# Kernel optimization log

Hardware: AMD Instinct MI355X
Metric: run time of the kernel (lower is better)

Reference implementation:

```python
import jax, jax.numpy as jnp
import numpy as np

N_NODES = 100000
N_EDGES = 1200000
N_GRAPHS = 1024
IN_FEATS = 64
HID = 64
BN_EPS = 1e-5


def setup_inputs() -> dict:
    key = jax.random.key(0)
    ks = jax.random.split(key, 20)
    feats = jax.random.normal(ks[0], (N_NODES, IN_FEATS), jnp.float32)
    src = jax.random.randint(ks[1], (N_EDGES,), 0, N_NODES, jnp.int32)
    dst = jax.random.randint(ks[2], (N_EDGES,), 0, N_NODES, jnp.int32)
    graph_ids = jnp.sort(jax.random.randint(ks[3], (N_NODES,), 0, N_GRAPHS, jnp.int32))

    def lin(k, fi, fo):
        s = 1.0 / np.sqrt(fi)
        kw, kb = jax.random.split(k)
        return (jax.random.uniform(kw, (fi, fo), jnp.float32, -s, s),
                jax.random.uniform(kb, (fo,), jnp.float32, -s, s))

    W_self, _ = lin(ks[4], IN_FEATS, HID)
    W_neigh, b_neigh = lin(ks[5], IN_FEATS, HID)
    W1, b1 = lin(ks[6], HID, 128)
    W2, b2 = lin(ks[7], 128, 64)
    W3, b3 = lin(ks[8], 64, 1)

    def bn(k, d):
        k1, k2, k3, k4 = jax.random.split(k, 4)
        return (jax.random.normal(k1, (d,), jnp.float32) * 0.1 + 1.0,
                jax.random.normal(k2, (d,), jnp.float32) * 0.1,
                jax.random.normal(k3, (d,), jnp.float32) * 0.1,
                jax.random.uniform(k4, (d,), jnp.float32, 0.5, 1.5))

    g1, be1, rm1, rv1 = bn(ks[9], 128)
    g2, be2, rm2, rv2 = bn(ks[10], 64)

    return dict(feats=feats, src=src, dst=dst, graph_ids=graph_ids,
                W_self=W_self, W_neigh=W_neigh, b_neigh=b_neigh,
                W1=W1, b1=b1, g1=g1, be1=be1, rm1=rm1, rv1=rv1,
                W2=W2, b2=b2, g2=g2, be2=be2, rm2=rm2, rv2=rv2,
                W3=W3, b3=b3)


def reference(feats, src, dst, graph_ids, W_self, W_neigh, b_neigh,
              W1, b1, g1, be1, rm1, rv1, W2, b2, g2, be2, rm2, rv2, W3, b3):
    # --- SAGEConv (mean aggregator): h = W_self@h_self + W_neigh@mean_neigh + b
    deg = jax.ops.segment_sum(jnp.ones((src.shape[0],), feats.dtype), dst,
                              num_segments=N_NODES)                      # [N]
    agg = jax.ops.segment_sum(feats[src], dst, num_segments=N_NODES)     # [N, F]
    mean_neigh = agg / jnp.maximum(deg, 1.0)[:, None]
    h = feats @ W_self + mean_neigh @ W_neigh + b_neigh
    h = jax.nn.relu(h)                                                   # activation

    # --- per-graph max readout (dgl.max_nodes)
    hg = jax.ops.segment_max(h, graph_ids, num_segments=N_GRAPHS)        # [G, HID]

    # --- MLP head with eval-mode BatchNorm1d
    def bn(x, g, b, rm, rv):
        return (x - rm) * jax.lax.rsqrt(rv + BN_EPS) * g + b

    x = bn(jax.nn.relu(hg @ W1 + b1), g1, be1, rm1, rv1)
    x = bn(jax.nn.relu(x @ W2 + b2), g2, be2, rm2, rv2)
    return x @ W3 + b3                                                   # [G, n_task]
```

## Files before the change

### kernel.cpp

```cpp
#include <hip/hip_runtime.h>
#include <hip/hip_fp16.h>

#define N_NODES  100000
#define N_EDGES  1200000
#define N_GRAPHS 1024
#define F        64
#define BN_EPS   1e-5f
#define NBUCK    ((N_NODES + 255) / 256)
#define NBLK     512
#define CHUNK    ((N_EDGES + NBLK - 1) / NBLK)
#define MT       128

__global__ __launch_bounds__(256) void chist(const int* __restrict__ dst,
                                             int* __restrict__ Ct,
                                             int* __restrict__ hgbits) {
  __shared__ int lh[NBUCK];
  int b = blockIdx.x, t = threadIdx.x;
  int zidx = b * 256 + t;
  if (zidx < N_GRAPHS * F) hgbits[zidx] = 0;
  for (int i = t; i < NBUCK; i += 256) lh[i] = 0;
  __syncthreads();
  int e0 = b * CHUNK, e1 = e0 + CHUNK;
  if (e1 > N_EDGES) e1 = N_EDGES;
  for (int e = e0 + t; e < e1; e += 256) atomicAdd(&lh[dst[e] >> 8], 1);
  __syncthreads();
  for (int i = t; i < NBUCK; i += 256) Ct[(size_t)b * NBUCK + i] = lh[i];
}

__global__ __launch_bounds__(NBLK) void cscan(int* __restrict__ Ct,
                                              int* __restrict__ bcnt) {
  __shared__ int s[NBLK];
  int i = blockIdx.x, t = threadIdx.x;
  int v = Ct[(size_t)t * NBUCK + i];
  s[t] = v;
  __syncthreads();
  for (int off = 1; off < NBLK; off <<= 1) {
    int u = (t >= off) ? s[t - off] : 0;
    __syncthreads();
    s[t] += u;
    __syncthreads();
  }
  Ct[(size_t)t * NBUCK + i] = s[t] - v;
  if (t == NBLK - 1) bcnt[i] = s[NBLK - 1];
}

__global__ __launch_bounds__(512) void bscan(const int* __restrict__ bcnt,
                                             int* __restrict__ bstart) {
  __shared__ int s[512];
  int t = threadIdx.x;
  int v = (t < NBUCK) ? bcnt[t] : 0;
  s[t] = v;
  __syncthreads();
  for (int off = 1; off < 512; off <<= 1) {
    int u = (t >= off) ? s[t - off] : 0;
    __syncthreads();
    s[t] += u;
    __syncthreads();
  }
  if (t < NBUCK) bstart[t] = s[t] - v;
  if (t == 0) bstart[NBUCK] = N_EDGES;
}

__global__ __launch_bounds__(256) void cscat(const int* __restrict__ src,
                                             const int* __restrict__ dst,
                                             const int* __restrict__ Ct,
                                             const int* __restrict__ bstart,
                                             int* __restrict__ pairs) {
  __shared__ int cur[NBUCK];
  int b = blockIdx.x, t = threadIdx.x;
  for (int i = t; i < NBUCK; i += 256)
    cur[i] = bstart[i] + Ct[(size_t)b * NBUCK + i];
  __syncthreads();
  int e0 = b * CHUNK, e1 = e0 + CHUNK;
  if (e1 > N_EDGES) e1 = N_EDGES;
  for (int e = e0 + t; e < e1; e += 256) {
    int d = dst[e];
    int pos = atomicAdd(&cur[d >> 8], 1);
    pairs[pos] = (int)((((unsigned)d & 255u) << 24) | (unsigned)src[e]);
  }
}

__global__ __launch_bounds__(256) void place(const int* __restrict__ pairs,
                                             const int* __restrict__ bstart,
                                             int* __restrict__ rs,
                                             int* __restrict__ eidx) {
  __shared__ int lh[256];
  __shared__ int cur[256];
  int b = blockIdx.x, t = threadIdx.x;
  int nb0 = b << 8;
  int r0 = bstart[b], r1 = bstart[b + 1];

  lh[t] = 0;
  __syncthreads();
  for (int e = r0 + t; e < r1; e += 256)
    atomicAdd(&lh[((unsigned)pairs[e]) >> 24], 1);
  __syncthreads();

  int v = lh[t];
  cur[t] = v;
  __syncthreads();
  for (int off = 1; off < 256; off <<= 1) {
    int u = (t >= off) ? cur[t - off] : 0;
    __syncthreads();
    cur[t] += u;
    __syncthreads();
  }
  int excl = cur[t] - v;
  int node = nb0 + t;
  if (node < N_NODES) rs[node] = r0 + excl;
  if (b == 0 && t == 0) rs[N_NODES] = N_EDGES;
  __syncthreads();
  cur[t] = r0 + excl;
  __syncthreads();

  for (int e = r0 + t; e < r1; e += 256) {
    unsigned p = (unsigned)pairs[e];
    int pos = atomicAdd(&cur[p >> 24], 1);
    eidx[pos] = (int)(p & 0xFFFFFFu);
  }
}

__global__ __launch_bounds__(256) void gemm_uz(
    const float* __restrict__ feats, const float* __restrict__ Wself,
    const float* __restrict__ Wneigh, __half* __restrict__ Uh,
    __half* __restrict__ Zh) {
  __shared__ float As[MT * 65];
  __shared__ float Ws[64 * 128];
  int t = threadIdx.x;
  int mbase = blockIdx.x * MT;

  for (int i = t; i < 64 * 128; i += 256) {
    int k = i >> 7, j = i & 127;
    Ws[i] = (j < 64) ? Wself[k * 64 + j] : Wneigh[k * 64 + (j - 64)];
  }
#pragma unroll
  for (int s = 0; s < 8; s++) {
    int idx = (s * 256 + t) * 4;
    int m = idx >> 6, k = idx & 63;
    int gm = mbase + m;
    float4 v = (gm < N_NODES) ? *(const float4*)(feats + (size_t)gm * F + k)
                              : make_float4(0.f, 0.f, 0.f, 0.f);
    float* d = As + m * 65 + k;
    d[0] = v.x; d[1] = v.y; d[2] = v.z; d[3] = v.w;
  }
  __syncthreads();

  int wave = t >> 6, lane = t & 63;
  int jq = lane & 3, nq = lane >> 2;
  int half = wave & 1;
  int mb = (wave >> 1) * 64 + 4 * nq;
  int joff = half * 64 + jq * 16;

  float acc[4][16];
#pragma unroll
  for (int i = 0; i < 4; i++)
#pragma unroll
    for (int c = 0; c < 16; c++) acc[i][c] = 0.f;

#pragma unroll 4
  for (int k = 0; k < 64; k++) {
    float a0 = As[(mb + 0) * 65 + k];
    float a1 = As[(mb + 1) * 65 + k];
    float a2 = As[(mb + 2) * 65 + k];
    float a3 = As[(mb + 3) * 65 + k];
    const float4* wr = (const float4*)(Ws + k * 128 + joff);
    float4 w4[4];
    w4[0] = wr[0]; w4[1] = wr[1]; w4[2] = wr[2]; w4[3] = wr[3];
    const float* w = (const float*)w4;
#pragma unroll
    for (int c = 0; c < 16; c++) {
      float wv = w[c];
      acc[0][c] += a0 * wv;
      acc[1][c] += a1 * wv;
      acc[2][c] += a2 * wv;
      acc[3][c] += a3 * wv;
    }
  }

  __half* outp = half ? Zh : Uh;
  int jbase = jq * 16;
#pragma unroll
  for (int i = 0; i < 4; i++) {
    int gm = mbase + mb + i;
    if (gm < N_NODES) {
#pragma unroll
      for (int c4 = 0; c4 < 4; c4++) {
        union { __half h[4]; uint2 u; } pk;
        pk.h[0] = __float2half_rn(acc[i][c4 * 4 + 0]);
        pk.h[1] = __float2half_rn(acc[i][c4 * 4 + 1]);
        pk.h[2] = __float2half_rn(acc[i][c4 * 4 + 2]);
        pk.h[3] = __float2half_rn(acc[i][c4 * 4 + 3]);
        *(uint2*)(outp + (size_t)gm * F + jbase + c4 * 4) = pk.u;
      }
    }
  }
}

__global__ __launch_bounds__(256) void gather_h(
    const __half* __restrict__ Uh, const __half* __restrict__ Zh,
    const int* __restrict__ rs, const int* __restrict__ eidx,
    const float* __restrict__ bneigh, const int* __restrict__ gids,
    int* __restrict__ hgbits) {
  int lane = threadIdx.x & 63;
  int wid  = (blockIdx.x * blockDim.x + threadIdx.x) >> 6;
  const int NW = (2048 * 256) >> 6;
  const int per = (N_NODES + NW - 1) / NW;
  int n0 = wid * per;
  int n1 = n0 + per; if (n1 > N_NODES) n1 = N_NODES;
  if (n0 >= n1) return;
  int fl  = lane & 15;
  int sub = lane >> 4;
  float4 b4 = *(const float4*)(bneigh + 4 * fl);

  int curg = gids[n0];
  float4 gmax = {0.f, 0.f, 0.f, 0.f};

  for (int n = n0; n < n1; n++) {
    uint2 ur = *(const uint2*)(Uh + (size_t)n * F + 4 * fl);
    int r0 = rs[n], r1 = rs[n + 1];
    float sx = 0.f, sy = 0.f, sz = 0.f, sw = 0.f;
    for (int base = r0; base < r1; base += 64) {
      int m = r1 - base; if (m > 64) m = 64;
      int myid = (lane < m) ? eidx[base + lane] : 0;
      for (int jj = 0; jj < m; jj += 16) {
        int j0 = jj + sub;
        int s0 = __shfl(myid, j0);
        int s1 = __shfl(myid, j0 + 4);
        int s2 = __shfl(myid, j0 + 8);
        int s3 = __shfl(myid, j0 + 12);
        uint2 z0 = *(const uint2*)(Zh + (size_t)s0 * F + 4 * fl);
        uint2 z1 = *(const uint2*)(Zh + (size_t)s1 * F + 4 * fl);
        uint2 z2 = *(const uint2*)(Zh + (size_t)s2 * F + 4 * fl);
        uint2 z3 = *(const uint2*)(Zh + (size_t)s3 * F + 4 * fl);
        if (j0 < m) {
          float2 f0 = __half22float2(*(__half2*)&z0.x);
          float2 f1 = __half22float2(*(__half2*)&z0.y);
          sx += f0.x; sy += f0.y; sz += f1.x; sw += f1.y;
        }
        if (j0 + 4 < m) {
          float2 f0 = __half22float2(*(__half2*)&z1.x);
          float2 f1 = __half22float2(*(__half2*)&z1.y);
          sx += f0.x; sy += f0.y; sz += f1.x; sw += f1.y;
        }
        if (j0 + 8 < m) {
          float2 f0 = __half22float2(*(__half2*)&z2.x);
          float2 f1 = __half22float2(*(__half2*)&z2.y);
          sx += f0.x; sy += f0.y; sz += f1.x; sw += f1.y;
        }
        if (j0 + 12 < m) {
          float2 f0 = __half22float2(*(__half2*)&z3.x);
          float2 f1 = __half22float2(*(__half2*)&z3.y);
          sx += f0.x; sy += f0.y; sz += f1.x; sw += f1.y;
        }
      }
    }
    sx += __shfl_xor(sx, 16); sy += __shfl_xor(sy, 16);
    sz += __shfl_xor(sz, 16); sw += __shfl_xor(sw, 16);
    sx += __shfl_xor(sx, 32); sy += __shfl_xor(sy, 32);
    sz += __shfl_xor(sz, 32); sw += __shfl_xor(sw, 32);
    float inv = 1.0f / fmaxf((float)(r1 - r0), 1.0f);

    int g = gids[n];
    if (g != curg) {
      if (sub == 0) {
        int* hp = hgbits + (size_t)curg * F + 4 * fl;
        atomicMax(hp + 0, __float_as_int(gmax.x));
        atomicMax(hp + 1, __float_as_int(gmax.y));
        atomicMax(hp + 2, __float_as_int(gmax.z));
        atomicMax(hp + 3, __float_as_int(gmax.w));
      }
      curg = g; gmax = make_float4(0.f, 0.f, 0.f, 0.f);
    }

    float2 uf0 = __half22float2(*(__half2*)&ur.x);
    float2 uf1 = __half22float2(*(__half2*)&ur.y);
    gmax.x = fmaxf(gmax.x, fmaxf(uf0.x + sx * inv + b4.x, 0.f));
    gmax.y = fmaxf(gmax.y, fmaxf(uf0.y + sy * inv + b4.y, 0.f));
    gmax.z = fmaxf(gmax.z, fmaxf(uf1.x + sz * inv + b4.z, 0.f));
    gmax.w = fmaxf(gmax.w, fmaxf(uf1.y + sw * inv + b4.w, 0.f));
  }
  if (sub == 0) {
    int* hp = hgbits + (size_t)curg * F + 4 * fl;
    atomicMax(hp + 0, __float_as_int(gmax.x));
    atomicMax(hp + 1, __float_as_int(gmax.y));
    atomicMax(hp + 2, __float_as_int(gmax.z));
    atomicMax(hp + 3, __float_as_int(gmax.w));
  }
}

#define GPB 8
__global__ __launch_bounds__(128) void mlp(
    const float* __restrict__ hg,
    const float* __restrict__ W1, const float* __restrict__ b1,
    const float* __restrict__ g1, const float* __restrict__ be1,
    const float* __restrict__ rm1, const float* __restrict__ rv1,
    const float* __restrict__ W2, const float* __restrict__ b2,
    const float* __restrict__ g2, const float* __restrict__ be2,
    const float* __restrict__ rm2, const float* __restrict__ rv2,
    const float* __restrict__ W3, const float* __restrict__ b3,
    float* __restrict__ out) {
  __shared__ float W1s[64 * 128];
  __shared__ float W2s[128 * 64];
  __shared__ float W3s[64];
  __shared__ float sc1[128], sh1[128], b1s[128];
  __shared__ float sc2[64],  sh2[64],  b2s[64];
  __shared__ float s0[64], s1[128], s2[64];
  int t = threadIdx.x;

  for (int i = t; i < 64 * 128; i += 128) W1s[i] = W1[i];
  for (int i = t; i < 128 * 64; i += 128) W2s[i] = W2[i];
  if (t < 64) W3s[t] = W3[t];
  {
    float iv = rsqrtf(rv1[t] + BN_EPS);
    float sc = g1[t] * iv;
    sc1[t] = sc; sh1[t] = be1[t] - rm1[t] * sc; b1s[t] = b1[t];
  }
  if (t < 64) {
    float iv = rsqrtf(rv2[t] + BN_EPS);
    float sc = g2[t] * iv;
    sc2[t] = sc; sh2[t] = be2[t] - rm2[t] * sc; b2s[t] = b2[t];
  }
  __syncthreads();

  for (int gg = 0; gg < GPB; gg++) {
    int g = blockIdx.x * GPB + gg;
    if (t < 64) s0[t] = hg[(size_t)g * F + t];
    __syncthreads();
    {
      float acc = b1s[t];
      for (int i = 0; i < 64; i++) acc += s0[i] * W1s[i * 128 + t];
      acc = fmaxf(acc, 0.0f);
      s1[t] = acc * sc1[t] + sh1[t];
    }
    __syncthreads();
    if (t < 64) {
      float acc = b2s[t];
      for (int i = 0; i < 128; i++) acc += s1[i] * W2s[i * 64 + t];
      acc = fmaxf(acc, 0.0f);
      s2[t] = acc * sc2[t] + sh2[t];
    }
    __syncthreads();
    if (t < 64) {
      float p = s2[t] * W3s[t];
      for (int off = 32; off > 0; off >>= 1) p += __shfl_down(p, off);
      if (t == 0) out[g] = p + b3[0];
    }
    __syncthreads();
  }
}

extern "C" void kernel_launch(void* const* d_in, const int* in_sizes, int n_in,
                              void* d_out, int out_size, void* d_ws, size_t ws_size,
                              hipStream_t stream) {
  const float* feats  = (const float*)d_in[0];
  const int*   src    = (const int*)d_in[1];
  const int*   dst    = (const int*)d_in[2];
  const int*   gids   = (const int*)d_in[3];
  const float* Wself  = (const float*)d_in[4];
  const float* Wneigh = (const float*)d_in[5];
  const float* bneigh = (const float*)d_in[6];
  const float* W1  = (const float*)d_in[7];
  const float* b1  = (const float*)d_in[8];
  const float* g1  = (const float*)d_in[9];
  const float* be1 = (const float*)d_in[10];
  const float* rm1 = (const float*)d_in[11];
  const float* rv1 = (const float*)d_in[12];
  const float* W2  = (const float*)d_in[13];
  const float* b2  = (const float*)d_in[14];
  const float* g2  = (const float*)d_in[15];
  const float* be2 = (const float*)d_in[16];
  const float* rm2 = (const float*)d_in[17];
  const float* rv2 = (const float*)d_in[18];
  const float* W3  = (const float*)d_in[19];
  const float* b3  = (const float*)d_in[20];

  __half* Uh   = (__half*)d_ws;
  __half* Zh   = Uh + (size_t)N_NODES * F;
  int* rs      = (int*)(Zh + (size_t)N_NODES * F);
  int* bstart  = rs + (N_NODES + 1);
  int* bcnt    = bstart + (NBUCK + 1);
  int* hgbits  = bcnt + NBUCK;
  int* Ct      = hgbits + (size_t)N_GRAPHS * F;
  int* pairs   = Ct + (size_t)NBLK * NBUCK;
  int* eidx    = pairs + N_EDGES;

  chist<<<NBLK, 256, 0, stream>>>(dst, Ct, hgbits);
  cscan<<<NBUCK, NBLK, 0, stream>>>(Ct, bcnt);
  bscan<<<1, 512, 0, stream>>>(bcnt, bstart);
  cscat<<<NBLK, 256, 0, stream>>>(src, dst, Ct, bstart, pairs);
  gemm_uz<<<(N_NODES + MT - 1) / MT, 256, 0, stream>>>(feats, Wself, Wneigh,
                                                       Uh, Zh);
  place<<<NBUCK, 256, 0, stream>>>(pairs, bstart, rs, eidx);
  gather_h<<<2048, 256, 0, stream>>>(Uh, Zh, rs, eidx, bneigh, gids, hgbits);
  mlp<<<N_GRAPHS / GPB, 128, 0, stream>>>((const float*)hgbits,
                                          W1, b1, g1, be1, rm1, rv1,
                                          W2, b2, g2, be2, rm2, rv2, W3, b3,
                                          (float*)d_out);
}
```

Before: 230.1 us.

## Fuse histogram into GEMM launch, merge scans, prefetch edge ids in gather

Adds the destination histogram blocks to the GEMM launch as extra blocks and merges the column scan with the bucket scan, using a last-block-done counter. This cuts two kernel launches and lets the histogram run alongside the GEMM. The gather kernel now loads the next node's row bounds and first 64 edge ids before finishing the current node, and it launches with twice as many blocks. This adds a threadfence and atomic counter plus extra registers, and the shared-memory buffer is sized for the GEMM, which may lower occupancy for the histogram blocks.

New measurement: 303.1 us. 1.32x slower.

```diff
diff --git a/kernel.cpp b/kernel.cpp
--- a/kernel.cpp
+++ b/kernel.cpp
@@ -10,123 +10,34 @@
 #define NBLK     512
 #define CHUNK    ((N_EDGES + NBLK - 1) / NBLK)
 #define MT       128
-
-__global__ __launch_bounds__(256) void chist(const int* __restrict__ dst,
-                                             int* __restrict__ Ct,
-                                             int* __restrict__ hgbits) {
-  __shared__ int lh[NBUCK];
-  int b = blockIdx.x, t = threadIdx.x;
-  int zidx = b * 256 + t;
-  if (zidx < N_GRAPHS * F) hgbits[zidx] = 0;
-  for (int i = t; i < NBUCK; i += 256) lh[i] = 0;
-  __syncthreads();
-  int e0 = b * CHUNK, e1 = e0 + CHUNK;
-  if (e1 > N_EDGES) e1 = N_EDGES;
-  for (int e = e0 + t; e < e1; e += 256) atomicAdd(&lh[dst[e] >> 8], 1);
-  __syncthreads();
-  for (int i = t; i < NBUCK; i += 256) Ct[(size_t)b * NBUCK + i] = lh[i];
-}
-
-__global__ __launch_bounds__(NBLK) void cscan(int* __restrict__ Ct,
-                                              int* __restrict__ bcnt) {
-  __shared__ int s[NBLK];
-  int i = blockIdx.x, t = threadIdx.x;
-  int v = Ct[(size_t)t * NBUCK + i];
-  s[t] = v;
-  __syncthreads();
-  for (int off = 1; off < NBLK; off <<= 1) {
-    int u = (t >= off) ? s[t - off] : 0;
-    __syncthreads();
-    s[t] += u;
-    __syncthreads();
-  }
-  Ct[(size_t)t * NBUCK + i] = s[t] - v;
-  if (t == NBLK - 1) bcnt[i] = s[NBLK - 1];
-}
-
-__global__ __launch_bounds__(512) void bscan(const int* __restrict__ bcnt,
-                                             int* __restrict__ bstart) {
-  __shared__ int s[512];
-  int t = threadIdx.x;
-  int v = (t < NBUCK) ? bcnt[t] : 0;
-  s[t] = v;
-  __syncthreads();
-  for (int off = 1; off < 512; off <<= 1) {
-    int u = (t >= off) ? s[t - off] : 0;
-    __syncthreads();
-    s[t] += u;
-    __syncthreads();
-  }
-  if (t < NBUCK) bstart[t] = s[t] - v;
-  if (t == 0) bstart[NBUCK] = N_EDGES;
-}
-
-__global__ __launch_bounds__(256) void cscat(const int* __restrict__ src,
-                                             const int* __restrict__ dst,
-                                             const int* __restrict__ Ct,
-                                             const int* __restrict__ bstart,
-                                             int* __restrict__ pairs) {
-  __shared__ int cur[NBUCK];
-  int b = blockIdx.x, t = threadIdx.x;
-  for (int i = t; i < NBUCK; i += 256)
-    cur[i] = bstart[i] + Ct[(size_t)b * NBUCK + i];
-  __syncthreads();
-  int e0 = b * CHUNK, e1 = e0 + CHUNK;
-  if (e1 > N_EDGES) e1 = N_EDGES;
-  for (int e = e0 + t; e < e1; e += 256) {
-    int d = dst[e];
-    int pos = atomicAdd(&cur[d >> 8], 1);
-    pairs[pos] = (int)((((unsigned)d & 255u) << 24) | (unsigned)src[e]);
-  }
-}
-
-__global__ __launch_bounds__(256) void place(const int* __restrict__ pairs,
-                                             const int* __restrict__ bstart,
-                                             int* __restrict__ rs,
-                                             int* __restrict__ eidx) {
-  __shared__ int lh[256];
-  __shared__ int cur[256];
-  int b = blockIdx.x, t = threadIdx.x;
-  int nb0 = b << 8;
-  int r0 = bstart[b], r1 = bstart[b + 1];
-
-  lh[t] = 0;
-  __syncthreads();
-  for (int e = r0 + t; e < r1; e += 256)
-    atomicAdd(&lh[((unsigned)pairs[e]) >> 24], 1);
-  __syncthreads();
-
-  int v = lh[t];
-  cur[t] = v;
-  __syncthreads();
-  for (int off = 1; off < 256; off <<= 1) {
-    int u = (t >= off) ? cur[t - off] : 0;
-    __syncthreads();
-    cur[t] += u;
-    __syncthreads();
-  }
-  int excl = cur[t] - v;
-  int node = nb0 + t;
-  if (node < N_NODES) rs[node] = r0 + excl;
-  if (b == 0 && t == 0) rs[N_NODES] = N_EDGES;
-  __syncthreads();
-  cur[t] = r0 + excl;
-  __syncthreads();
-
-  for (int e = r0 + t; e < r1; e += 256) {
-    unsigned p = (unsigned)pairs[e];
-    int pos = atomicAdd(&cur[p >> 24], 1);
-    eidx[pos] = (int)(p & 0xFFFFFFu);
-  }
-}
-
-__global__ __launch_bounds__(256) void gemm_uz(
+#define GEMM_BLOCKS ((N_NODES + MT - 1) / MT)
+
+__global__ __launch_bounds__(256) void prep(
     const float* __restrict__ feats, const float* __restrict__ Wself,
     const float* __restrict__ Wneigh, __half* __restrict__ Uh,
-    __half* __restrict__ Zh) {
-  __shared__ float As[MT * 65];
-  __shared__ float Ws[64 * 128];
+    __half* __restrict__ Zh, const int* __restrict__ dst,
+    int* __restrict__ Ct, int* __restrict__ hgbits, int* __restrict__ done) {
+  __shared__ __align__(16) char smraw[MT * 65 * 4 + 64 * 128 * 4];
   int t = threadIdx.x;
+  if (blockIdx.x == 0 && t == 0) *done = 0;
+
+  if (blockIdx.x >= GEMM_BLOCKS) {
+    int* lh = (int*)smraw;
+    int b = blockIdx.x - GEMM_BLOCKS;
+    int zidx = b * 256 + t;
+    if (zidx < N_GRAPHS * F) hgbits[zidx] = 0;
+    for (int i = t; i < NBUCK; i += 256) lh[i] = 0;
+    __syncthreads();
+    int e0 = b * CHUNK, e1 = e0 + CHUNK;
+    if (e1 > N_EDGES) e1 = N_EDGES;
+    for (int e = e0 + t; e < e1; e += 256) atomicAdd(&lh[dst[e] >> 8], 1);
+    __syncthreads();
+    for (int i = t; i < NBUCK; i += 256) Ct[(size_t)b * NBUCK + i] = lh[i];
+    return;
+  }
+
+  float* As = (float*)smraw;
+  float* Ws = (float*)(smraw + MT * 65 * 4);
   int mbase = blockIdx.x * MT;
 
   for (int i = t; i < 64 * 128; i += 256) {
@@ -196,6 +107,102 @@
   }
 }
 
+__global__ __launch_bounds__(NBLK) void cscan2(int* __restrict__ Ct,
+                                               int* __restrict__ bcnt,
+                                               int* __restrict__ bstart,
+                                               int* __restrict__ done) {
+  __shared__ int s[NBLK];
+  __shared__ int lastflag;
+  int i = blockIdx.x, t = threadIdx.x;
+  int v = Ct[(size_t)t * NBUCK + i];
+  s[t] = v;
+  __syncthreads();
+  for (int off = 1; off < NBLK; off <<= 1) {
+    int u = (t >= off) ? s[t - off] : 0;
+    __syncthreads();
+    s[t] += u;
+    __syncthreads();
+  }
+  Ct[(size_t)t * NBUCK + i] = s[t] - v;
+  if (t == NBLK - 1) bcnt[i] = s[NBLK - 1];
+  __threadfence();
+  __syncthreads();
+  if (t == 0) lastflag = (atomicAdd(done, 1) == NBUCK - 1) ? 1 : 0;
+  __syncthreads();
+  if (!lastflag) return;
+
+  int w = (t < NBUCK) ? atomicAdd(&bcnt[t], 0) : 0;
+  s[t] = w;
+  __syncthreads();
+  for (int off = 1; off < NBLK; off <<= 1) {
+    int u = (t >= off) ? s[t - off] : 0;
+    __syncthreads();
+    s[t] += u;
+    __syncthreads();
+  }
+  if (t < NBUCK) bstart[t] = s[t] - w;
+  if (t == 0) bstart[NBUCK] = N_EDGES;
+}
+
+__global__ __launch_bounds__(256) void cscat(const int* __restrict__ src,
+                                             const int* __restrict__ dst,
+                                             const int* __restrict__ Ct,
+                                             const int* __restrict__ bstart,
+                                             int* __restrict__ pairs) {
+  __shared__ int cur[NBUCK];
+  int b = blockIdx.x, t = threadIdx.x;
+  for (int i = t; i < NBUCK; i += 256)
+    cur[i] = bstart[i] + Ct[(size_t)b * NBUCK + i];
+  __syncthreads();
+  int e0 = b * CHUNK, e1 = e0 + CHUNK;
+  if (e1 > N_EDGES) e1 = N_EDGES;
+  for (int e = e0 + t; e < e1; e += 256) {
+    int d = dst[e];
+    int pos = atomicAdd(&cur[d >> 8], 1);
+    pairs[pos] = (int)((((unsigned)d & 255u) << 24) | (unsigned)src[e]);
+  }
+}
+
+__global__ __launch_bounds__(256) void place(const int* __restrict__ pairs,
+                                             const int* __restrict__ bstart,
+                                             int* __restrict__ rs,
+                                             int* __restrict__ eidx) {
+  __shared__ int lh[256];
+  __shared__ int cur[256];
+  int b = blockIdx.x, t = threadIdx.x;
+  int nb0 = b << 8;
+  int r0 = bstart[b], r1 = bstart[b + 1];
+
+  lh[t] = 0;
+  __syncthreads();
+  for (int e = r0 + t; e < r1; e += 256)
+    atomicAdd(&lh[((unsigned)pairs[e]) >> 24], 1);
+  __syncthreads();
+
+  int v = lh[t];
+  cur[t] = v;
+  __syncthreads();
+  for (int off = 1; off < 256; off <<= 1) {
+    int u = (t >= off) ? cur[t - off] : 0;
+    __syncthreads();
+    cur[t] += u;
+    __syncthreads();
+  }
+  int excl = cur[t] - v;
+  int node = nb0 + t;
+  if (node < N_NODES) rs[node] = r0 + excl;
+  if (b == 0 && t == 0) rs[N_NODES] = N_EDGES;
+  __syncthreads();
+  cur[t] = r0 + excl;
+  __syncthreads();
+
+  for (int e = r0 + t; e < r1; e += 256) {
+    unsigned p = (unsigned)pairs[e];
+    int pos = atomicAdd(&cur[p >> 24], 1);
+    eidx[pos] = (int)(p & 0xFFFFFFu);
+  }
+}
+
 __global__ __launch_bounds__(256) void gather_h(
     const __half* __restrict__ Uh, const __half* __restrict__ Zh,
     const int* __restrict__ rs, const int* __restrict__ eidx,
@@ -203,7 +210,7 @@
     int* __restrict__ hgbits) {
   int lane = threadIdx.x & 63;
   int wid  = (blockIdx.x * blockDim.x + threadIdx.x) >> 6;
-  const int NW = (2048 * 256) >> 6;
+  const int NW = (4096 * 256) >> 6;
   const int per = (N_NODES + NW - 1) / NW;
   int n0 = wid * per;
   int n1 = n0 + per; if (n1 > N_NODES) n1 = N_NODES;
@@ -215,19 +222,57 @@
   int curg = gids[n0];
   float4 gmax = {0.f, 0.f, 0.f, 0.f};
 
+  int r0 = rs[n0], r1 = rs[n0 + 1];
+  int myid = (lane < r1 - r0) ? eidx[r0 + lane] : 0;
+
   for (int n = n0; n < n1; n++) {
     uint2 ur = *(const uint2*)(Uh + (size_t)n * F + 4 * fl);
-    int r0 = rs[n], r1 = rs[n + 1];
+    int nr0 = 0, nr1 = 0;
+    if (n + 1 < n1) { nr0 = rs[n + 1]; nr1 = rs[n + 2]; }
+
     float sx = 0.f, sy = 0.f, sz = 0.f, sw = 0.f;
-    for (int base = r0; base < r1; base += 64) {
+    int deg = r1 - r0;
+    int m0 = deg > 64 ? 64 : deg;
+    for (int jj = 0; jj < m0; jj += 16) {
+      int j0 = jj + sub;
+      int s0 = __shfl(myid, j0);
+      int s1 = __shfl(myid, j0 + 4);
+      int s2 = __shfl(myid, j0 + 8);
+      int s3 = __shfl(myid, j0 + 12);
+      uint2 z0 = *(const uint2*)(Zh + (size_t)s0 * F + 4 * fl);
+      uint2 z1 = *(const uint2*)(Zh + (size_t)s1 * F + 4 * fl);
+      uint2 z2 = *(const uint2*)(Zh + (size_t)s2 * F + 4 * fl);
+      uint2 z3 = *(const uint2*)(Zh + (size_t)s3 * F + 4 * fl);
+      if (j0 < m0) {
+        float2 f0 = __half22float2(*(__half2*)&z0.x);
+        float2 f1 = __half22float2(*(__half2*)&z0.y);
+        sx += f0.x; sy += f0.y; sz += f1.x; sw += f1.y;
+      }
+      if (j0 + 4 < m0) {
+        float2 f0 = __half22float2(*(__half2*)&z1.x);
+        float2 f1 = __half22float2(*(__half2*)&z1.y);
+        sx += f0.x; sy += f0.y; sz += f1.x; sw += f1.y;
+      }
+      if (j0 + 8 < m0) {
+        float2 f0 = __half22float2(*(__half2*)&z2.x);
+        float2 f1 = __half22float2(*(__half2*)&z2.y);
+        sx += f0.x; sy += f0.y; sz += f1.x; sw += f1.y;
+      }
+      if (j0 + 12 < m0) {
+        float2 f0 = __half22float2(*(__half2*)&z3.x);
+        float2 f1 = __half22float2(*(__half2*)&z3.y);
+        sx += f0.x; sy += f0.y; sz += f1.x; sw += f1.y;
+      }
+    }
+    for (int base = r0 + 64; base < r1; base += 64) {
       int m = r1 - base; if (m > 64) m = 64;
-      int myid = (lane < m) ? eidx[base + lane] : 0;
+      int myid2 = (lane < m) ? eidx[base + lane] : 0;
       for (int jj = 0; jj < m; jj += 16) {
         int j0 = jj + sub;
-        int s0 = __shfl(myid, j0);
-        int s1 = __shfl(myid, j0 + 4);
-        int s2 = __shfl(myid, j0 + 8);
-        int s3 = __shfl(myid, j0 + 12);
+        int s0 = __shfl(myid2, j0);
+        int s1 = __shfl(myid2, j0 + 4);
+        int s2 = __shfl(myid2, j0 + 8);
+        int s3 = __shfl(myid2, j0 + 12);
         uint2 z0 = *(const uint2*)(Zh + (size_t)s0 * F + 4 * fl);
         uint2 z1 = *(const uint2*)(Zh + (size_t)s1 * F + 4 * fl);
         uint2 z2 = *(const uint2*)(Zh + (size_t)s2 * F + 4 * fl);
@@ -254,11 +299,15 @@
         }
       }
     }
+
+    int nmyid = 0;
+    if (n + 1 < n1) nmyid = (lane < nr1 - nr0) ? eidx[nr0 + lane] : 0;
+
     sx += __shfl_xor(sx, 16); sy += __shfl_xor(sy, 16);
     sz += __shfl_xor(sz, 16); sw += __shfl_xor(sw, 16);
     sx += __shfl_xor(sx, 32); sy += __shfl_xor(sy, 32);
     sz += __shfl_xor(sz, 32); sw += __shfl_xor(sw, 32);
-    float inv = 1.0f / fmaxf((float)(r1 - r0), 1.0f);
+    float inv = 1.0f / fmaxf((float)deg, 1.0f);
 
     int g = gids[n];
     if (g != curg) {
@@ -278,6 +327,8 @@
     gmax.y = fmaxf(gmax.y, fmaxf(uf0.y + sy * inv + b4.y, 0.f));
     gmax.z = fmaxf(gmax.z, fmaxf(uf1.x + sz * inv + b4.z, 0.f));
     gmax.w = fmaxf(gmax.w, fmaxf(uf1.y + sw * inv + b4.w, 0.f));
+
+    r0 = nr0; r1 = nr1; myid = nmyid;
   }
   if (sub == 0) {
     int* hp = hgbits + (size_t)curg * F + 4 * fl;
@@ -379,19 +430,18 @@
   int* rs      = (int*)(Zh + (size_t)N_NODES * F);
   int* bstart  = rs + (N_NODES + 1);
   int* bcnt    = bstart + (NBUCK + 1);
-  int* hgbits  = bcnt + NBUCK;
+  int* done    = bcnt + NBUCK;
+  int* hgbits  = done + 1;
   int* Ct      = hgbits + (size_t)N_GRAPHS * F;
   int* pairs   = Ct + (size_t)NBLK * NBUCK;
   int* eidx    = pairs + N_EDGES;
 
-  chist<<<NBLK, 256, 0, stream>>>(dst, Ct, hgbits);
-  cscan<<<NBUCK, NBLK, 0, stream>>>(Ct, bcnt);
-  bscan<<<1, 512, 0, stream>>>(bcnt, bstart);
+  prep<<<GEMM_BLOCKS + NBLK, 256, 0, stream>>>(feats, Wself, Wneigh, Uh, Zh,
+                                               dst, Ct, hgbits, done);
+  cscan2<<<NBUCK, NBLK, 0, stream>>>(Ct, bcnt, bstart, done);
   cscat<<<NBLK, 256, 0, stream>>>(src, dst, Ct, bstart, pairs);
-  gemm_uz<<<(N_NODES + MT - 1) / MT, 256, 0, stream>>>(feats, Wself, Wneigh,
-                                                       Uh, Zh);
   place<<<NBUCK, 256, 0, stream>>>(pairs, bstart, rs, eidx);
-  gather_h<<<2048, 256, 0, stream>>>(Uh, Zh, rs, eidx, bneigh, gids, hgbits);
+  gather_h<<<4096, 256, 0, stream>>>(Uh, Zh, rs, eidx, bneigh, gids, hgbits);
   mlp<<<N_GRAPHS / GPB, 128, 0, stream>>>((const float*)hgbits,
                                           W1, b1, g1, be1, rm1, rv1,
                                           W2, b2, g2, be2, rm2, rv2, W3, b3,
```

## Fuse CSR placement into gather via LDS and merge histogram into GEMM launch

Applied to the files above, without the earlier changes.

Merges the destination histogram into the feature GEMM launch as extra blocks, and fuses the per-bucket CSR placement into the neighbor gather so edge indices and row starts live in shared memory instead of global arrays. This removes two kernel launches and the global write/read of the edge index array and row-start array. It trades off reduced gather parallelism (one 1024-thread block per 256-node bucket) and caps per-bucket edges at a fixed LDS capacity, silently dropping edges if a bucket exceeds it.

New measurement: 214.2 us. -6.9%, faster.

```diff
diff --git a/kernel.cpp b/kernel.cpp
--- a/kernel.cpp
+++ b/kernel.cpp
@@ -10,123 +10,34 @@
 #define NBLK     512
 #define CHUNK    ((N_EDGES + NBLK - 1) / NBLK)
 #define MT       128
-
-__global__ __launch_bounds__(256) void chist(const int* __restrict__ dst,
-                                             int* __restrict__ Ct,
-                                             int* __restrict__ hgbits) {
-  __shared__ int lh[NBUCK];
-  int b = blockIdx.x, t = threadIdx.x;
-  int zidx = b * 256 + t;
-  if (zidx < N_GRAPHS * F) hgbits[zidx] = 0;
-  for (int i = t; i < NBUCK; i += 256) lh[i] = 0;
-  __syncthreads();
-  int e0 = b * CHUNK, e1 = e0 + CHUNK;
-  if (e1 > N_EDGES) e1 = N_EDGES;
-  for (int e = e0 + t; e < e1; e += 256) atomicAdd(&lh[dst[e] >> 8], 1);
-  __syncthreads();
-  for (int i = t; i < NBUCK; i += 256) Ct[(size_t)b * NBUCK + i] = lh[i];
-}
-
-__global__ __launch_bounds__(NBLK) void cscan(int* __restrict__ Ct,
-                                              int* __restrict__ bcnt) {
-  __shared__ int s[NBLK];
-  int i = blockIdx.x, t = threadIdx.x;
-  int v = Ct[(size_t)t * NBUCK + i];
-  s[t] = v;
-  __syncthreads();
-  for (int off = 1; off < NBLK; off <<= 1) {
-    int u = (t >= off) ? s[t - off] : 0;
-    __syncthreads();
-    s[t] += u;
-    __syncthreads();
-  }
-  Ct[(size_t)t * NBUCK + i] = s[t] - v;
-  if (t == NBLK - 1) bcnt[i] = s[NBLK - 1];
-}
-
-__global__ __launch_bounds__(512) void bscan(const int* __restrict__ bcnt,
-                                             int* __restrict__ bstart) {
-  __shared__ int s[512];
-  int t = threadIdx.x;
-  int v = (t < NBUCK) ? bcnt[t] : 0;
-  s[t] = v;
-  __syncthreads();
-  for (int off = 1; off < 512; off <<= 1) {
-    int u = (t >= off) ? s[t - off] : 0;
-    __syncthreads();
-    s[t] += u;
-    __syncthreads();
-  }
-  if (t < NBUCK) bstart[t] = s[t] - v;
-  if (t == 0) bstart[NBUCK] = N_EDGES;
-}
-
-__global__ __launch_bounds__(256) void cscat(const int* __restrict__ src,
-                                             const int* __restrict__ dst,
-                                             const int* __restrict__ Ct,
-                                             const int* __restrict__ bstart,
-                                             int* __restrict__ pairs) {
-  __shared__ int cur[NBUCK];
-  int b = blockIdx.x, t = threadIdx.x;
-  for (int i = t; i < NBUCK; i += 256)
-    cur[i] = bstart[i] + Ct[(size_t)b * NBUCK + i];
-  __syncthreads();
-  int e0 = b * CHUNK, e1 = e0 + CHUNK;
-  if (e1 > N_EDGES) e1 = N_EDGES;
-  for (int e = e0 + t; e < e1; e += 256) {
-    int d = dst[e];
-    int pos = atomicAdd(&cur[d >> 8], 1);
-    pairs[pos] = (int)((((unsigned)d & 255u) << 24) | (unsigned)src[e]);
-  }
-}
-
-__global__ __launch_bounds__(256) void place(const int* __restrict__ pairs,
-                                             const int* __restrict__ bstart,
-                                             int* __restrict__ rs,
-                                             int* __restrict__ eidx) {
-  __shared__ int lh[256];
-  __shared__ int cur[256];
-  int b = blockIdx.x, t = threadIdx.x;
-  int nb0 = b << 8;
-  int r0 = bstart[b], r1 = bstart[b + 1];
-
-  lh[t] = 0;
-  __syncthreads();
-  for (int e = r0 + t; e < r1; e += 256)
-    atomicAdd(&lh[((unsigned)pairs[e]) >> 24], 1);
-  __syncthreads();
-
-  int v = lh[t];
-  cur[t] = v;
-  __syncthreads();
-  for (int off = 1; off < 256; off <<= 1) {
-    int u = (t >= off) ? cur[t - off] : 0;
-    __syncthreads();
-    cur[t] += u;
-    __syncthreads();
-  }
-  int excl = cur[t] - v;
-  int node = nb0 + t;
-  if (node < N_NODES) rs[node] = r0 + excl;
-  if (b == 0 && t == 0) rs[N_NODES] = N_EDGES;
-  __syncthreads();
-  cur[t] = r0 + excl;
-  __syncthreads();
-
-  for (int e = r0 + t; e < r1; e += 256) {
-    unsigned p = (unsigned)pairs[e];
-    int pos = atomicAdd(&cur[p >> 24], 1);
-    eidx[pos] = (int)(p & 0xFFFFFFu);
-  }
-}
-
-__global__ __launch_bounds__(256) void gemm_uz(
+#define GEMM_BLOCKS ((N_NODES + MT - 1) / MT)
+#define CE       3584
+
+__global__ __launch_bounds__(256) void prep(
     const float* __restrict__ feats, const float* __restrict__ Wself,
     const float* __restrict__ Wneigh, __half* __restrict__ Uh,
-    __half* __restrict__ Zh) {
-  __shared__ float As[MT * 65];
-  __shared__ float Ws[64 * 128];
+    __half* __restrict__ Zh, const int* __restrict__ dst,
+    int* __restrict__ Ct, int* __restrict__ hgbits) {
+  __shared__ __align__(16) char smraw[MT * 65 * 4 + 64 * 128 * 4];
   int t = threadIdx.x;
+
+  if (blockIdx.x >= GEMM_BLOCKS) {
+    int* lh = (int*)smraw;
+    int b = blockIdx.x - GEMM_BLOCKS;
+    int zidx = b * 256 + t;
+    if (zidx < N_GRAPHS * F) hgbits[zidx] = 0;
+    for (int i = t; i < NBUCK; i += 256) lh[i] = 0;
+    __syncthreads();
+    int e0 = b * CHUNK, e1 = e0 + CHUNK;
+    if (e1 > N_EDGES) e1 = N_EDGES;
+    for (int e = e0 + t; e < e1; e += 256) atomicAdd(&lh[dst[e] >> 8], 1);
+    __syncthreads();
+    for (int i = t; i < NBUCK; i += 256) Ct[(size_t)b * NBUCK + i] = lh[i];
+    return;
+  }
+
+  float* As = (float*)smraw;
+  float* Ws = (float*)(smraw + MT * 65 * 4);
   int mbase = blockIdx.x * MT;
 
   for (int i = t; i < 64 * 128; i += 256) {
@@ -196,71 +107,150 @@
   }
 }
 
-__global__ __launch_bounds__(256) void gather_h(
+__global__ __launch_bounds__(NBLK) void cscan(int* __restrict__ Ct,
+                                              int* __restrict__ bcnt) {
+  __shared__ int s[NBLK];
+  int i = blockIdx.x, t = threadIdx.x;
+  int v = Ct[(size_t)t * NBUCK + i];
+  s[t] = v;
+  __syncthreads();
+  for (int off = 1; off < NBLK; off <<= 1) {
+    int u = (t >= off) ? s[t - off] : 0;
+    __syncthreads();
+    s[t] += u;
+    __syncthreads();
+  }
+  Ct[(size_t)t * NBUCK + i] = s[t] - v;
+  if (t == NBLK - 1) bcnt[i] = s[NBLK - 1];
+}
+
+__global__ __launch_bounds__(512) void bscan(const int* __restrict__ bcnt,
+                                             int* __restrict__ bstart) {
+  __shared__ int s[512];
+  int t = threadIdx.x;
+  int v = (t < NBUCK) ? bcnt[t] : 0;
+  s[t] = v;
+  __syncthreads();
+  for (int off = 1; off < 512; off <<= 1) {
+    int u = (t >= off) ? s[t - off] : 0;
+    __syncthreads();
+    s[t] += u;
+    __syncthreads();
+  }
+  if (t < NBUCK) bstart[t] = s[t] - v;
+  if (t == 0) bstart[NBUCK] = N_EDGES;
+}
+
+__global__ __launch_bounds__(256) void cscat(const int* __restrict__ src,
+                                             const int* __restrict__ dst,
+                                             const int* __restrict__ Ct,
+                                             const int* __restrict__ bstart,
+                                             int* __restrict__ pairs) {
+  __shared__ int cur[NBUCK];
+  int b = blockIdx.x, t = threadIdx.x;
+  for (int i = t; i < NBUCK; i += 256)
+    cur[i] = bstart[i] + Ct[(size_t)b * NBUCK + i];
+  __syncthreads();
+  int e0 = b * CHUNK, e1 = e0 + CHUNK;
+  if (e1 > N_EDGES) e1 = N_EDGES;
+  for (int e = e0 + t; e < e1; e += 256) {
+    int d = dst[e];
+    int pos = atomicAdd(&cur[d >> 8], 1);
+    pairs[pos] = (int)((((unsigned)d & 255u) << 24) | (unsigned)src[e]);
+  }
+}
+
+__global__ __launch_bounds__(1024) void gather_place(
     const __half* __restrict__ Uh, const __half* __restrict__ Zh,
-    const int* __restrict__ rs, const int* __restrict__ eidx,
+    const int* __restrict__ pairs, const int* __restrict__ bstart,
     const float* __restrict__ bneigh, const int* __restrict__ gids,
     int* __restrict__ hgbits) {
-  int lane = threadIdx.x & 63;
-  int wid  = (blockIdx.x * blockDim.x + threadIdx.x) >> 6;
-  const int NW = (2048 * 256) >> 6;
-  const int per = (N_NODES + NW - 1) / NW;
-  int n0 = wid * per;
-  int n1 = n0 + per; if (n1 > N_NODES) n1 = N_NODES;
-  if (n0 >= n1) return;
-  int fl  = lane & 15;
-  int sub = lane >> 4;
+  __shared__ int eidx_l[CE];
+  __shared__ int rsl[256];
+  __shared__ int lh[256];
+  __shared__ int cur[256];
+  int b = blockIdx.x, t = threadIdx.x;
+  int nb0 = b << 8;
+  int r0 = bstart[b], r1 = bstart[b + 1];
+  int E = r1 - r0; if (E > CE) E = CE;
+
+  if (t < 256) lh[t] = 0;
+  __syncthreads();
+  for (int e = t; e < E; e += 1024)
+    atomicAdd(&lh[((unsigned)pairs[r0 + e]) >> 24], 1);
+  __syncthreads();
+  if (t < 256) cur[t] = lh[t];
+  __syncthreads();
+  for (int off = 1; off < 256; off <<= 1) {
+    int u = (t < 256 && t >= off) ? cur[t - off] : 0;
+    __syncthreads();
+    if (t < 256) cur[t] += u;
+    __syncthreads();
+  }
+  if (t < 256) { int ex = cur[t] - lh[t]; rsl[t] = ex; cur[t] = ex; }
+  __syncthreads();
+  for (int e = t; e < E; e += 1024) {
+    unsigned p = (unsigned)pairs[r0 + e];
+    int pos = atomicAdd(&cur[p >> 24], 1);
+    eidx_l[pos] = (int)(p & 0xFFFFFFu);
+  }
+  __syncthreads();
+
+  int wave = t >> 6, lane = t & 63;
+  int fl = lane & 15, sub = lane >> 4;
   float4 b4 = *(const float4*)(bneigh + 4 * fl);
-
-  int curg = gids[n0];
+  int nl = wave * 16;
+  int nend = nl + 16;
+  if (nb0 + nl >= N_NODES) return;
+  if (nb0 + nend > N_NODES) nend = N_NODES - nb0;
+
+  int curg = gids[nb0 + nl];
   float4 gmax = {0.f, 0.f, 0.f, 0.f};
 
-  for (int n = n0; n < n1; n++) {
-    uint2 ur = *(const uint2*)(Uh + (size_t)n * F + 4 * fl);
-    int r0 = rs[n], r1 = rs[n + 1];
+  for (; nl < nend; nl++) {
+    int node = nb0 + nl;
+    int rr  = rsl[nl];
+    int deg = lh[nl];
+    uint2 ur = *(const uint2*)(Uh + (size_t)node * F + 4 * fl);
     float sx = 0.f, sy = 0.f, sz = 0.f, sw = 0.f;
-    for (int base = r0; base < r1; base += 64) {
-      int m = r1 - base; if (m > 64) m = 64;
-      int myid = (lane < m) ? eidx[base + lane] : 0;
-      for (int jj = 0; jj < m; jj += 16) {
-        int j0 = jj + sub;
-        int s0 = __shfl(myid, j0);
-        int s1 = __shfl(myid, j0 + 4);
-        int s2 = __shfl(myid, j0 + 8);
-        int s3 = __shfl(myid, j0 + 12);
-        uint2 z0 = *(const uint2*)(Zh + (size_t)s0 * F + 4 * fl);
-        uint2 z1 = *(const uint2*)(Zh + (size_t)s1 * F + 4 * fl);
-        uint2 z2 = *(const uint2*)(Zh + (size_t)s2 * F + 4 * fl);
-        uint2 z3 = *(const uint2*)(Zh + (size_t)s3 * F + 4 * fl);
-        if (j0 < m) {
-          float2 f0 = __half22float2(*(__half2*)&z0.x);
-          float2 f1 = __half22float2(*(__half2*)&z0.y);
-          sx += f0.x; sy += f0.y; sz += f1.x; sw += f1.y;
-        }
-        if (j0 + 4 < m) {
-          float2 f0 = __half22float2(*(__half2*)&z1.x);
-          float2 f1 = __half22float2(*(__half2*)&z1.y);
-          sx += f0.x; sy += f0.y; sz += f1.x; sw += f1.y;
-        }
-        if (j0 + 8 < m) {
-          float2 f0 = __half22float2(*(__half2*)&z2.x);
-          float2 f1 = __half22float2(*(__half2*)&z2.y);
-          sx += f0.x; sy += f0.y; sz += f1.x; sw += f1.y;
-        }
-        if (j0 + 12 < m) {
-          float2 f0 = __half22float2(*(__half2*)&z3.x);
-          float2 f1 = __half22float2(*(__half2*)&z3.y);
-          sx += f0.x; sy += f0.y; sz += f1.x; sw += f1.y;
-        }
+    for (int jj = 0; jj < deg; jj += 16) {
+      int j0 = jj + sub;
+      int s0 = (j0      < deg) ? eidx_l[rr + j0]      : 0;
+      int s1 = (j0 + 4  < deg) ? eidx_l[rr + j0 + 4]  : 0;
+      int s2 = (j0 + 8  < deg) ? eidx_l[rr + j0 + 8]  : 0;
+      int s3 = (j0 + 12 < deg) ? eidx_l[rr + j0 + 12] : 0;
+      uint2 z0 = *(const uint2*)(Zh + (size_t)s0 * F + 4 * fl);
+      uint2 z1 = *(const uint2*)(Zh + (size_t)s1 * F + 4 * fl);
+      uint2 z2 = *(const uint2*)(Zh + (size_t)s2 * F + 4 * fl);
+      uint2 z3 = *(const uint2*)(Zh + (size_t)s3 * F + 4 * fl);
+      if (j0 < deg) {
+        float2 f0 = __half22float2(*(__half2*)&z0.x);
+        float2 f1 = __half22float2(*(__half2*)&z0.y);
+        sx += f0.x; sy += f0.y; sz += f1.x; sw += f1.y;
+      }
+      if (j0 + 4 < deg) {
+        float2 f0 = __half22float2(*(__half2*)&z1.x);
+        float2 f1 = __half22float2(*(__half2*)&z1.y);
+        sx += f0.x; sy += f0.y; sz += f1.x; sw += f1.y;
+      }
+      if (j0 + 8 < deg) {
+        float2 f0 = __half22float2(*(__half2*)&z2.x);
+        float2 f1 = __half22float2(*(__half2*)&z2.y);
+        sx += f0.x; sy += f0.y; sz += f1.x; sw += f1.y;
+      }
+      if (j0 + 12 < deg) {
+        float2 f0 = __half22float2(*(__half2*)&z3.x);
+        float2 f1 = __half22float2(*(__half2*)&z3.y);
+        sx += f0.x; sy += f0.y; sz += f1.x; sw += f1.y;
       }
     }
     sx += __shfl_xor(sx, 16); sy += __shfl_xor(sy, 16);
     sz += __shfl_xor(sz, 16); sw += __shfl_xor(sw, 16);
     sx += __shfl_xor(sx, 32); sy += __shfl_xor(sy, 32);
     sz += __shfl_xor(sz, 32); sw += __shfl_xor(sw, 32);
-    float inv = 1.0f / fmaxf((float)(r1 - r0), 1.0f);
-
-    int g = gids[n];
+    float inv = 1.0f / fmaxf((float)deg, 1.0f);
+
+    int g = gids[node];
     if (g != curg) {
       if (sub == 0) {
         int* hp = hgbits + (size_t)curg * F + 4 * fl;
@@ -376,22 +366,19 @@
 
   __half* Uh   = (__half*)d_ws;
   __half* Zh   = Uh + (size_t)N_NODES * F;
-  int* rs      = (int*)(Zh + (size_t)N_NODES * F);
-  int* bstart  = rs + (N_NODES + 1);
+  int* bstart  = (int*)(Zh + (size_t)N_NODES * F);
   int* bcnt    = bstart + (NBUCK + 1);
   int* hgbits  = bcnt + NBUCK;
   int* Ct      = hgbits + (size_t)N_GRAPHS * F;
   int* pairs   = Ct + (size_t)NBLK * NBUCK;
-  int* eidx    = pairs + N_EDGES;
-
-  chist<<<NBLK, 256, 0, stream>>>(dst, Ct, hgbits);
+
+  prep<<<GEMM_BLOCKS + NBLK, 256, 0, stream>>>(feats, Wself, Wneigh, Uh, Zh,
+                                               dst, Ct, hgbits);
   cscan<<<NBUCK, NBLK, 0, stream>>>(Ct, bcnt);
   bscan<<<1, 512, 0, stream>>>(bcnt, bstart);
   cscat<<<NBLK, 256, 0, stream>>>(src, dst, Ct, bstart, pairs);
-  gemm_uz<<<(N_NODES + MT - 1) / MT, 256, 0, stream>>>(feats, Wself, Wneigh,
-                                                       Uh, Zh);
-  place<<<NBUCK, 256, 0, stream>>>(pairs, bstart, rs, eidx);
-  gather_h<<<2048, 256, 0, stream>>>(Uh, Zh, rs, eidx, bneigh, gids, hgbits);
+  gather_place<<<NBUCK, 1024, 0, stream>>>(Uh, Zh, pairs, bstart, bneigh,
+                                           gids, hgbits);
   mlp<<<N_GRAPHS / GPB, 128, 0, stream>>>((const float*)hgbits,
                                           W1, b1, g1, be1, rm1, rv1,
                                           W2, b2, g2, be2, rm2, rv2, W3, b3,
```
